# Performance work log

Hardware: AMD Instinct MI355X
Metric: run time of the kernel (lower is better)

Reference implementation:

```python
import jax, jax.numpy as jnp
import numpy as np
from jax import lax

RADIUS = 0.3
NSAMPLE = 16
NPOINT = 1024
NH = 1   # num_heading_bin
NS = 18  # num_size_cluster
EPS = 1e-5  # torch BatchNorm eps


def _bn(x, g, b, m, v):
    # eval-mode batchnorm over the last (channel) axis
    return (x - m) * (g / jnp.sqrt(v + EPS)) + b


def _fps(xyz, npoint):
    # furthest point sampling; xyz: (B,K,3) -> (B,npoint) int32 indices
    B, K, _ = xyz.shape
    def body(carry, _):
        dists, far = carry
        cur = jnp.take_along_axis(xyz, far[:, None, None], axis=1)  # (B,1,3)
        d = jnp.sum((xyz - cur) ** 2, -1)                           # (B,K)
        dists = jnp.minimum(dists, d)
        nxt = jnp.argmax(dists, -1).astype(jnp.int32)
        return (dists, nxt), far
    init = (jnp.full((B, K), 1e10, xyz.dtype), jnp.zeros((B,), jnp.int32))
    _, inds = lax.scan(body, init, None, length=npoint)
    return jnp.swapaxes(inds, 0, 1)  # (B, npoint)


def _ball_query(xyz, new_xyz):
    # first-NSAMPLE points within RADIUS of each center, pad with first hit
    K = xyz.shape[1]
    d2 = jnp.sum((new_xyz[:, :, None, :] - xyz[:, None, :, :]) ** 2, -1)  # (B,S,K)
    mask = d2 < RADIUS ** 2
    idx = jnp.where(mask, jnp.arange(K, dtype=jnp.int32)[None, None, :], K)
    idx = jnp.sort(idx, -1)[..., :NSAMPLE]
    first = idx[..., :1]
    idx = jnp.where(idx == K, first, idx)
    idx = jnp.where(idx == K, 0, idx)  # degenerate: no neighbor at all
    return idx  # (B,S,NSAMPLE)


def setup_inputs() -> dict:
    key = jax.random.key(0)
    ks = jax.random.split(key, 32)
    inp = {}
    inp['xyz'] = jax.random.normal(ks[0], (8, 8192, 3), jnp.float32)
    inp['features'] = jax.random.normal(ks[1], (8, 256, 8192), jnp.float32)
    i = 2
    # shared MLP: 259 -> 128 -> 128 -> 128 (conv2d 1x1, no bias, then BN)
    for l, (o, c) in enumerate([(128, 259), (128, 128), (128, 128)]):
        inp[f'mlp_w{l}'] = jax.random.normal(ks[i], (o, c), jnp.float32) * 0.1; i += 1
        inp[f'mlp_g{l}'] = jnp.ones((o,), jnp.float32)
        inp[f'mlp_b{l}'] = jnp.zeros((o,), jnp.float32)
        inp[f'mlp_m{l}'] = jax.random.normal(ks[i], (o,), jnp.float32) * 0.01; i += 1
        inp[f'mlp_v{l}'] = jax.random.uniform(ks[i], (o,), jnp.float32, 0.5, 1.5); i += 1
    # box head convs (conv1d k=1)
    for nm, (o, c) in [('c1', (128, 128)), ('c2', (128, 128)), ('c3', (97, 128))]:
        inp[f'{nm}_w'] = jax.random.normal(ks[i], (o, c), jnp.float32) * 0.1; i += 1
        inp[f'{nm}_b'] = jnp.zeros((o,), jnp.float32)
    for nm in ['bn1', 'bn2']:
        inp[f'{nm}_g'] = jnp.ones((128,), jnp.float32)
        inp[f'{nm}_b'] = jnp.zeros((128,), jnp.float32)
        inp[f'{nm}_m'] = jax.random.normal(ks[i], (128,), jnp.float32) * 0.01; i += 1
        inp[f'{nm}_v'] = jax.random.uniform(ks[i], (128,), jnp.float32, 0.5, 1.5); i += 1
    inp['mean_size_arr'] = jax.random.uniform(ks[i], (NS, 3), jnp.float32, 0.3, 2.0)
    return inp


def reference(xyz, features,
              mlp_w0, mlp_g0, mlp_b0, mlp_m0, mlp_v0,
              mlp_w1, mlp_g1, mlp_b1, mlp_m1, mlp_v1,
              mlp_w2, mlp_g2, mlp_b2, mlp_m2, mlp_v2,
              c1_w, c1_b, bn1_g, bn1_b, bn1_m, bn1_v,
              c2_w, c2_b, bn2_g, bn2_b, bn2_m, bn2_v,
              c3_w, c3_b, mean_size_arr):
    B = xyz.shape[0]
    # --- vote aggregation: FPS + ball query + group + shared MLP + maxpool ---
    fps_inds = _fps(xyz, NPOINT)
    new_xyz = jnp.take_along_axis(xyz, fps_inds[..., None], axis=1)  # (B,S,3)
    idx = _ball_query(xyz, new_xyz)                                  # (B,S,n)
    gather = jax.vmap(lambda a, i: a[i])
    g_xyz = (gather(xyz, idx) - new_xyz[:, :, None, :]) / RADIUS     # normalize_xyz
    g_f = gather(jnp.swapaxes(features, 1, 2), idx)                  # (B,S,n,256)
    h = jnp.concatenate([g_xyz, g_f], -1)                            # (B,S,n,259)
    for w, g, b, m, v in ((mlp_w0, mlp_g0, mlp_b0, mlp_m0, mlp_v0),
                          (mlp_w1, mlp_g1, mlp_b1, mlp_m1, mlp_v1),
                          (mlp_w2, mlp_g2, mlp_b2, mlp_m2, mlp_v2)):
        h = jax.nn.relu(_bn(jnp.einsum('bsnc,oc->bsno', h, w), g, b, m, v))
    feat = jnp.max(h, axis=2)                                        # (B,S,128)
    # --- box head (conv1d k=1 == per-point linear) ---
    net = jax.nn.relu(_bn(jnp.einsum('bsc,oc->bso', feat, c1_w) + c1_b,
                          bn1_g, bn1_b, bn1_m, bn1_v))
    net = jax.nn.relu(_bn(jnp.einsum('bsc,oc->bso', net, c2_w) + c2_b,
                          bn2_g, bn2_b, bn2_m, bn2_v))
    net = jnp.einsum('bsc,oc->bso', net, c3_w) + c3_b                # (B,S,97)
    # --- decode_scores ---
    obj = net[..., 0:2]
    center = new_xyz + net[..., 2:5]
    hs = net[..., 5:5 + NH]
    hr = net[..., 5 + NH:5 + 2 * NH] * (np.pi / NH)
    ss = net[..., 5 + 2 * NH:5 + 2 * NH + NS]
    srn = net[..., 5 + 2 * NH + NS:5 + 2 * NH + 4 * NS].reshape(B, NPOINT, NS, 3)
    sr = (srn * mean_size_arr[None, None]).reshape(B, NPOINT, NS * 3)
    sem = net[..., 5 + 2 * NH + 4 * NS:]
    return jnp.concatenate([obj, center, hs, hr, ss, sr, sem], -1)   # (B,S,97)
```

## Files before the change

### kernel.cpp

```cpp
#include <hip/hip_runtime.h>
#include <cstdint>
#include <cstddef>

#define BATCH   8
#define KPTS    8192
#define NPT     1024
#define NSAMP   16
#define RAD2    0.09f

typedef float f32x2 __attribute__((ext_vector_type(2)));
typedef float f32x4 __attribute__((ext_vector_type(4)));
typedef short s16x4 __attribute__((ext_vector_type(4)));
typedef short s16x8 __attribute__((ext_vector_type(8)));

__device__ __forceinline__ unsigned short f2bf(float x) {
    unsigned u = __float_as_uint(x);
    return (unsigned short)((u + 0x7fffu + ((u >> 16) & 1u)) >> 16);
}

template <int CTRL>
__device__ __forceinline__ unsigned long long dpp_max_step(unsigned long long v) {
    unsigned int lo = (unsigned int)v, hi = (unsigned int)(v >> 32);
    unsigned int lo2 = (unsigned int)__builtin_amdgcn_update_dpp(0, (int)lo, CTRL, 0xf, 0xf, true);
    unsigned int hi2 = (unsigned int)__builtin_amdgcn_update_dpp(0, (int)hi, CTRL, 0xf, 0xf, true);
    unsigned long long o = ((unsigned long long)hi2 << 32) | lo2;
    return o > v ? o : v;
}

__global__ __launch_bounds__(512, 1) void fps_f0_kernel(
    const float* __restrict__ xyz, float* __restrict__ new_xyz,
    const float* __restrict__ feats, const float* __restrict__ w0,
    float* __restrict__ f0out) {
    __shared__ float xs[KPTS], ys[KPTS], zs[KPTS];
    __shared__ __align__(16) unsigned long long wslot[2][8];
    __shared__ int   hist[NPT];
    __shared__ float As[16 * 128];
    __shared__ float Bs[16 * 130];

    const int tid = threadIdx.x;

    if (blockIdx.x >= 8) {
        const int bid = blockIdx.x - 8;
        const int b   = bid >> 6;
        const int p0  = (bid & 63) << 7;
        const int rb  = (tid >> 4) << 2;
        const int ob  = tid & 15;
        const float* fb = feats + (size_t)b * 256 * KPTS;

        float acc[4][8];
#pragma unroll
        for (int r = 0; r < 4; ++r)
#pragma unroll
            for (int c = 0; c < 8; ++c) acc[r][c] = 0.f;

        for (int k0 = 0; k0 < 256; k0 += 16) {
#pragma unroll
            for (int i = 0; i < 4; ++i) {
                int e = tid + (i << 9);
                int kk = e >> 7, pc = e & 127;
                As[kk * 128 + pc] = fb[(size_t)(k0 + kk) * KPTS + p0 + pc];
            }
#pragma unroll
            for (int i = 0; i < 4; ++i) {
                int e = tid + (i << 9);
                int o = e >> 4, kk = e & 15;
                Bs[kk * 130 + o] = w0[o * 259 + 3 + k0 + kk];
            }
            __syncthreads();
#pragma unroll
            for (int kk = 0; kk < 16; ++kk) {
                float a[4], wvv[8];
#pragma unroll
                for (int r = 0; r < 4; ++r) a[r] = As[kk * 128 + rb + r];
#pragma unroll
                for (int c = 0; c < 8; ++c) wvv[c] = Bs[kk * 130 + ob + (c << 4)];
#pragma unroll
                for (int r = 0; r < 4; ++r)
#pragma unroll
                    for (int c = 0; c < 8; ++c) acc[r][c] = fmaf(a[r], wvv[c], acc[r][c]);
            }
            __syncthreads();
        }
#pragma unroll
        for (int r = 0; r < 4; ++r) {
            float* outp = f0out + ((size_t)b * KPTS + p0 + rb + r) * 128 + ob;
#pragma unroll
            for (int c = 0; c < 8; ++c) outp[c << 4] = acc[r][c];
        }
        return;
    }

    {
#pragma clang fp contract(off)
        const int b = blockIdx.x;
        const float* xb = xyz + (size_t)b * KPTS * 3;

        for (int i = tid; i < KPTS; i += 512) {
            xs[i] = xb[i * 3 + 0];
            ys[i] = xb[i * 3 + 1];
            zs[i] = xb[i * 3 + 2];
        }
        __syncthreads();

        const int base = tid << 4;
        f32x2 px[8], py[8], pz[8], dmn[8];
#pragma unroll
        for (int j = 0; j < 8; ++j) {
            int i0 = base + (j << 1);
            px[j] = (f32x2){xs[i0], xs[i0 + 1]};
            py[j] = (f32x2){ys[i0], ys[i0 + 1]};
            pz[j] = (f32x2){zs[i0], zs[i0 + 1]};
            dmn[j] = (f32x2){1e10f, 1e10f};
        }

        int far = 0;
        for (int it = 0; it < NPT; ++it) {
            if (tid == 0) hist[it] = far;
            const float cx = xs[far], cy = ys[far], cz = zs[far];
            const f32x2 cx2 = (f32x2){cx, cx};
            const f32x2 cy2 = (f32x2){cy, cy};
            const f32x2 cz2 = (f32x2){cz, cz};

            f32x2 mm = (f32x2){-1.0f, -1.0f};
#pragma unroll
            for (int j = 0; j < 8; ++j) {
                f32x2 dx = px[j] - cx2;
                f32x2 dy = py[j] - cy2;
                f32x2 dz = pz[j] - cz2;
                f32x2 d  = (dx * dx + dy * dy) + dz * dz;
                f32x2 nd = __builtin_elementwise_min(dmn[j], d);
                dmn[j] = nd;
                mm = __builtin_elementwise_max(mm, nd);
            }
            float lmax = fmaxf(mm.x, mm.y);

            int ci = 0x7fffffff;
#pragma unroll
            for (int j = 0; j < 8; ++j) {
                if (dmn[j].x == lmax) ci = min(ci, base + (j << 1));
                if (dmn[j].y == lmax) ci = min(ci, base + (j << 1) + 1);
            }

            unsigned long long pk =
                ((unsigned long long)__float_as_uint(lmax) << 32) | (unsigned)(8191 - ci);

            pk = dpp_max_step<0x111>(pk);
            pk = dpp_max_step<0x112>(pk);
            pk = dpp_max_step<0x114>(pk);
            pk = dpp_max_step<0x118>(pk);
            pk = dpp_max_step<0x142>(pk);
            pk = dpp_max_step<0x143>(pk);

            if ((tid & 63) == 63) wslot[it & 1][tid >> 6] = pk;
            __syncthreads();

            ulonglong2 s01 = *(const ulonglong2*)&wslot[it & 1][0];
            ulonglong2 s23 = *(const ulonglong2*)&wslot[it & 1][2];
            ulonglong2 s45 = *(const ulonglong2*)&wslot[it & 1][4];
            ulonglong2 s67 = *(const ulonglong2*)&wslot[it & 1][6];
            unsigned long long g = s01.x;
            if (s01.y > g) g = s01.y;
            if (s23.x > g) g = s23.x;
            if (s23.y > g) g = s23.y;
            if (s45.x > g) g = s45.x;
            if (s45.y > g) g = s45.y;
            if (s67.x > g) g = s67.x;
            if (s67.y > g) g = s67.y;
            far = 8191 - (int)(unsigned)(g & 0xffffffffull);
        }

        for (int i = tid; i < NPT; i += 512) {
            int idx = hist[i];
            float* o = new_xyz + ((size_t)b * NPT + i) * 3;
            o[0] = xs[idx]; o[1] = ys[idx]; o[2] = zs[idx];
        }
    }
}

__global__ __launch_bounds__(256) void ballq_kernel(const float* __restrict__ xyz,
                                                    const float* __restrict__ new_xyz,
                                                    int* __restrict__ idxout) {
    const int tid  = threadIdx.x;
    const int lane = tid & 63;
    const int q    = (blockIdx.x << 2) + (tid >> 6);
    const int b    = q >> 10;
    const float* xb = xyz + (size_t)b * KPTS * 3;
    const float qx = new_xyz[q * 3 + 0];
    const float qy = new_xyz[q * 3 + 1];
    const float qz = new_xyz[q * 3 + 2];
    int* op = idxout + q * NSAMP;

    int total = 0;
    int first_p = 0;
    for (int c = 0; c < KPTS / 64; ++c) {
        int p = (c << 6) + lane;
        float pxv = xb[p * 3 + 0], pyv = xb[p * 3 + 1], pzv = xb[p * 3 + 2];
        float dx = __fsub_rn(qx, pxv), dy = __fsub_rn(qy, pyv), dz = __fsub_rn(qz, pzv);
        float d2 = __fadd_rn(__fadd_rn(__fmul_rn(dx, dx), __fmul_rn(dy, dy)),
                             __fmul_rn(dz, dz));
        bool pred = d2 < RAD2;
        unsigned long long mask = __ballot(pred);
        if (total == 0 && mask != 0ull) first_p = (c << 6) + (int)__builtin_ctzll(mask);
        if (pred) {
            int rank = (int)__popcll(mask & ((1ull << lane) - 1ull));
            int slot = total + rank;
            if (slot < NSAMP) op[slot] = p;
        }
        total += (int)__popcll(mask);
        if (total >= NSAMP) break;
    }
    if (total < NSAMP && lane >= total && lane < NSAMP) op[lane] = first_p;
}

#define HB 136

__global__ __launch_bounds__(256) void mlp_kernel(
    const float* __restrict__ f0, const int* __restrict__ idxw,
    const float* __restrict__ xyz, const float* __restrict__ new_xyz,
    const float* __restrict__ w0,
    const float* __restrict__ g0, const float* __restrict__ b0,
    const float* __restrict__ m0, const float* __restrict__ v0,
    const float* __restrict__ w1,
    const float* __restrict__ g1, const float* __restrict__ b1a,
    const float* __restrict__ m1, const float* __restrict__ v1,
    const float* __restrict__ w2,
    const float* __restrict__ g2, const float* __restrict__ b2a,
    const float* __restrict__ m2, const float* __restrict__ v2,
    float* __restrict__ featout) {
    const int tid = threadIdx.x;
    const int q0  = blockIdx.x << 2;
    const int b   = q0 >> 10;

    __shared__ __align__(16) unsigned short hbf[64 * HB];
    __shared__ __align__(16) unsigned short Wsh[128 * HB];
    __shared__ float gx[64], gy[64], gz[64];
    __shared__ int   pidx[64];
    __shared__ float s0[128], t0[128], wxs[128], wys[128], wzs[128];
    __shared__ float s1[128], t1[128], s2[128], t2[128];

    if (tid < 64) pidx[tid] = idxw[(q0 + (tid >> 4)) * NSAMP + (tid & 15)];
    if (tid < 128) {
        float sc = g0[tid] / sqrtf(v0[tid] + 1e-5f);
        s0[tid] = sc; t0[tid] = b0[tid] - m0[tid] * sc;
        sc = g1[tid] / sqrtf(v1[tid] + 1e-5f);
        s1[tid] = sc; t1[tid] = b1a[tid] - m1[tid] * sc;
        sc = g2[tid] / sqrtf(v2[tid] + 1e-5f);
        s2[tid] = sc; t2[tid] = b2a[tid] - m2[tid] * sc;
        wxs[tid] = w0[tid * 259 + 0];
        wys[tid] = w0[tid * 259 + 1];
        wzs[tid] = w0[tid * 259 + 2];
    }
    __syncthreads();
    if (tid < 64) {
        int p = pidx[tid];
        int q = q0 + (tid >> 4);
        const float* pp = xyz + ((size_t)b * KPTS + p) * 3;
        const float* nq = new_xyz + (size_t)q * 3;
        gx[tid] = (pp[0] - nq[0]) / 0.3f;
        gy[tid] = (pp[1] - nq[1]) / 0.3f;
        gz[tid] = (pp[2] - nq[2]) / 0.3f;
    }
    __syncthreads();

#pragma unroll 2
    for (int i = 0; i < 8; ++i) {
        int e = tid + (i << 8);
        int row = e >> 5, o = (e & 31) << 2;
        int p = pidx[row];
        float4 v4 = *(const float4*)(f0 + ((size_t)b * KPTS + p) * 128 + o);
        float gxr = gx[row], gyr = gy[row], gzr = gz[row];
        float r0 = fmaf(wzs[o + 0], gzr, fmaf(wys[o + 0], gyr, fmaf(wxs[o + 0], gxr, v4.x)));
        float r1 = fmaf(wzs[o + 1], gzr, fmaf(wys[o + 1], gyr, fmaf(wxs[o + 1], gxr, v4.y)));
        float r2 = fmaf(wzs[o + 2], gzr, fmaf(wys[o + 2], gyr, fmaf(wxs[o + 2], gxr, v4.z)));
        float r3 = fmaf(wzs[o + 3], gzr, fmaf(wys[o + 3], gyr, fmaf(wxs[o + 3], gxr, v4.w)));
        s16x4 c4;
        c4.x = (short)f2bf(fmaxf(fmaf(r0, s0[o + 0], t0[o + 0]), 0.f));
        c4.y = (short)f2bf(fmaxf(fmaf(r1, s0[o + 1], t0[o + 1]), 0.f));
        c4.z = (short)f2bf(fmaxf(fmaf(r2, s0[o + 2], t0[o + 2]), 0.f));
        c4.w = (short)f2bf(fmaxf(fmaf(r3, s0[o + 3], t0[o + 3]), 0.f));
        *(s16x4*)&hbf[row * HB + o] = c4;
    }
#pragma unroll 4
    for (int i = 0; i < 16; ++i) {
        int e = tid + (i << 8);
        int o = e >> 5;
        int kt = (e & 31) << 2;
        float4 w4 = *(const float4*)(w1 + o * 128 + kt);
        s16x4 c4 = { (short)f2bf(w4.x), (short)f2bf(w4.y),
                     (short)f2bf(w4.z), (short)f2bf(w4.w) };
        *(s16x4*)&Wsh[o * HB + kt] = c4;
    }
    __syncthreads();

    const int w    = tid >> 6;
    const int lane = tid & 63;
    const int l15  = lane & 15;
    const int quad = lane >> 4;
    const int wrow = w << 4;

    f32x4 acc[8];
#pragma unroll
    for (int t = 0; t < 8; ++t) acc[t] = (f32x4){0.f, 0.f, 0.f, 0.f};
#pragma unroll
    for (int k0 = 0; k0 < 128; k0 += 32) {
        s16x8 a = *(const s16x8*)&hbf[(wrow + l15) * HB + k0 + (quad << 3)];
#pragma unroll
        for (int t = 0; t < 8; ++t) {
            s16x8 bf = *(const s16x8*)&Wsh[((t << 4) + l15) * HB + k0 + (quad << 3)];
            acc[t] = __builtin_amdgcn_mfma_f32_16x16x32_bf16(a, bf, acc[t], 0, 0, 0);
        }
    }
    __syncthreads();

#pragma unroll
    for (int t = 0; t < 8; ++t) {
        int o = (t << 4) + l15;
        float ss = s1[o], tt = t1[o];
#pragma unroll
        for (int r = 0; r < 4; ++r) {
            float v = fmaxf(fmaf(acc[t][r], ss, tt), 0.f);
            hbf[(wrow + (quad << 2) + r) * HB + o] = f2bf(v);
        }
    }
#pragma unroll 4
    for (int i = 0; i < 16; ++i) {
        int e = tid + (i << 8);
        int o = e >> 5;
        int kt = (e & 31) << 2;
        float4 w4 = *(const float4*)(w2 + o * 128 + kt);
        s16x4 c4 = { (short)f2bf(w4.x), (short)f2bf(w4.y),
                     (short)f2bf(w4.z), (short)f2bf(w4.w) };
        *(s16x4*)&Wsh[o * HB + kt] = c4;
    }
    __syncthreads();

#pragma unroll
    for (int t = 0; t < 8; ++t) acc[t] = (f32x4){0.f, 0.f, 0.f, 0.f};
#pragma unroll
    for (int k0 = 0; k0 < 128; k0 += 32) {
        s16x8 a = *(const s16x8*)&hbf[(wrow + l15) * HB + k0 + (quad << 3)];
#pragma unroll
        for (int t = 0; t < 8; ++t) {
            s16x8 bf = *(const s16x8*)&Wsh[((t << 4) + l15) * HB + k0 + (quad << 3)];
            acc[t] = __builtin_amdgcn_mfma_f32_16x16x32_bf16(a, bf, acc[t], 0, 0, 0);
        }
    }

#pragma unroll
    for (int t = 0; t < 8; ++t) {
        int o = (t << 4) + l15;
        float ss = s2[o], tt = t2[o];
        float m0v = fmaxf(fmaf(acc[t][0], ss, tt), 0.f);
        float m1v = fmaxf(fmaf(acc[t][1], ss, tt), 0.f);
        float m2v = fmaxf(fmaf(acc[t][2], ss, tt), 0.f);
        float m3v = fmaxf(fmaf(acc[t][3], ss, tt), 0.f);
        float m = fmaxf(fmaxf(m0v, m1v), fmaxf(m2v, m3v));
        m = fmaxf(m, __shfl_xor(m, 16));
        m = fmaxf(m, __shfl_xor(m, 32));
        if (quad == 0)
            featout[(size_t)(q0 + w) * 128 + o] = m;
    }
}

__global__ __launch_bounds__(256) void head_kernel(
    const float* __restrict__ feat, const float* __restrict__ new_xyz,
    const float* __restrict__ c1w, const float* __restrict__ c1b,
    const float* __restrict__ c2w, const float* __restrict__ c2b,
    const float* __restrict__ c3w, const float* __restrict__ c3b,
    const float* __restrict__ bg1, const float* __restrict__ bb1,
    const float* __restrict__ bm1, const float* __restrict__ bv1,
    const float* __restrict__ bg2, const float* __restrict__ bb2,
    const float* __restrict__ bm2, const float* __restrict__ bv2,
    const float* __restrict__ msz, float* __restrict__ out) {
    const int tid = threadIdx.x;
    const int q0  = blockIdx.x << 3;
    __shared__ float fs[8][128], n1[8][128], n2[8][128];
    __shared__ float s1[128], t1[128], s2[128], t2[128], ms[54];

#pragma unroll
    for (int i = 0; i < 4; ++i) {
        int e = tid + (i << 8);
        fs[e >> 7][e & 127] = feat[(size_t)q0 * 128 + e];
    }
    if (tid < 128) {
        float sc = bg1[tid] / sqrtf(bv1[tid] + 1e-5f);
        s1[tid] = sc; t1[tid] = bb1[tid] - bm1[tid] * sc;
        sc = bg2[tid] / sqrtf(bv2[tid] + 1e-5f);
        s2[tid] = sc; t2[tid] = bb2[tid] - bm2[tid] * sc;
    }
    if (tid < 54) ms[tid] = msz[tid];
    __syncthreads();

    const int o    = tid & 127;
    const int half = tid >> 7;

    {
        float a[4];
#pragma unroll
        for (int j = 0; j < 4; ++j) a[j] = c1b[o];
        const float* wr = c1w + o * 128;
        for (int k = 0; k < 128; k += 4) {
            float4 w4 = *(const float4*)(wr + k);
#pragma unroll
            for (int j = 0; j < 4; ++j) {
                int qq = half * 4 + j;
                a[j] = fmaf(fs[qq][k + 0], w4.x, a[j]);
                a[j] = fmaf(fs[qq][k + 1], w4.y, a[j]);
                a[j] = fmaf(fs[qq][k + 2], w4.z, a[j]);
                a[j] = fmaf(fs[qq][k + 3], w4.w, a[j]);
            }
        }
#pragma unroll
        for (int j = 0; j < 4; ++j)
            n1[half * 4 + j][o] = fmaxf(fmaf(a[j], s1[o], t1[o]), 0.f);
    }
    __syncthreads();
    {
        float a[4];
#pragma unroll
        for (int j = 0; j < 4; ++j) a[j] = c2b[o];
        const float* wr = c2w + o * 128;
        for (int k = 0; k < 128; k += 4) {
            float4 w4 = *(const float4*)(wr + k);
#pragma unroll
            for (int j = 0; j < 4; ++j) {
                int qq = half * 4 + j;
                a[j] = fmaf(n1[qq][k + 0], w4.x, a[j]);
                a[j] = fmaf(n1[qq][k + 1], w4.y, a[j]);
                a[j] = fmaf(n1[qq][k + 2], w4.z, a[j]);
                a[j] = fmaf(n1[qq][k + 3], w4.w, a[j]);
            }
        }
#pragma unroll
        for (int j = 0; j < 4; ++j)
            n2[half * 4 + j][o] = fmaxf(fmaf(a[j], s2[o], t2[o]), 0.f);
    }
    __syncthreads();
    if (o < 97) {
        float a[4];
#pragma unroll
        for (int j = 0; j < 4; ++j) a[j] = c3b[o];
        const float* wr = c3w + o * 128;
        for (int k = 0; k < 128; k += 4) {
            float4 w4 = *(const float4*)(wr + k);
#pragma unroll
            for (int j = 0; j < 4; ++j) {
                int qq = half * 4 + j;
                a[j] = fmaf(n2[qq][k + 0], w4.x, a[j]);
                a[j] = fmaf(n2[qq][k + 1], w4.y, a[j]);
                a[j] = fmaf(n2[qq][k + 2], w4.z, a[j]);
                a[j] = fmaf(n2[qq][k + 3], w4.w, a[j]);
            }
        }
#pragma unroll
        for (int j = 0; j < 4; ++j) {
            int q = q0 + half * 4 + j;
            float v = a[j];
            if (o >= 2 && o < 5) v += new_xyz[(size_t)q * 3 + (o - 2)];
            else if (o == 6) v *= 3.14159265358979323846f;
            else if (o >= 25 && o < 79) v *= ms[o - 25];
            out[(size_t)q * 97 + o] = v;
        }
    }
}

extern "C" void kernel_launch(void* const* d_in, const int* in_sizes, int n_in,
                              void* d_out, int out_size, void* d_ws, size_t ws_size,
                              hipStream_t stream) {
    const float* xyz      = (const float*)d_in[0];
    const float* features = (const float*)d_in[1];
    const float* w0  = (const float*)d_in[2];
    const float* g0  = (const float*)d_in[3];
    const float* b0  = (const float*)d_in[4];
    const float* m0  = (const float*)d_in[5];
    const float* v0  = (const float*)d_in[6];
    const float* w1  = (const float*)d_in[7];
    const float* g1  = (const float*)d_in[8];
    const float* b1  = (const float*)d_in[9];
    const float* m1  = (const float*)d_in[10];
    const float* v1  = (const float*)d_in[11];
    const float* w2  = (const float*)d_in[12];
    const float* g2  = (const float*)d_in[13];
    const float* b2  = (const float*)d_in[14];
    const float* m2  = (const float*)d_in[15];
    const float* v2  = (const float*)d_in[16];
    const float* c1w = (const float*)d_in[17];
    const float* c1b = (const float*)d_in[18];
    const float* c2w = (const float*)d_in[19];
    const float* c2b = (const float*)d_in[20];
    const float* c3w = (const float*)d_in[21];
    const float* c3b = (const float*)d_in[22];
    const float* bg1 = (const float*)d_in[23];
    const float* bb1 = (const float*)d_in[24];
    const float* bm1 = (const float*)d_in[25];
    const float* bv1 = (const float*)d_in[26];
    const float* bg2 = (const float*)d_in[27];
    const float* bb2 = (const float*)d_in[28];
    const float* bm2 = (const float*)d_in[29];
    const float* bv2 = (const float*)d_in[30];
    const float* msz = (const float*)d_in[31];

    float* F0   = (float*)d_ws;
    float* feat = F0 + (size_t)BATCH * KPTS * 128;
    int*   idxw = (int*)(feat + (size_t)BATCH * NPT * 128);
    float* nxyz = (float*)(idxw + (size_t)BATCH * NPT * NSAMP);
    float* outp = (float*)d_out;

    fps_f0_kernel<<<8 + BATCH * (KPTS / 128), 512, 0, stream>>>(
        xyz, nxyz, features, w0, F0);
    ballq_kernel<<<BATCH * NPT / 4, 256, 0, stream>>>(xyz, nxyz, idxw);
    mlp_kernel  <<<BATCH * NPT / 4, 256, 0, stream>>>(
        F0, idxw, xyz, nxyz, w0, g0, b0, m0, v0,
        w1, g1, b1, m1, v1, w2, g2, b2, m2, v2, feat);
    head_kernel <<<BATCH * NPT / 8, 256, 0, stream>>>(
        feat, nxyz, c1w, c1b, c2w, c2b, c3w, c3b,
        bg1, bb1, bm1, bv1, bg2, bb2, bm2, bv2, msz, outp);
}
```

Before: 1.248 ms.

## Shrink FPS block to 256 threads, reduce argmax via float DPP and LDS atomicMax

```diff
diff --git a/kernel.cpp b/kernel.cpp
--- a/kernel.cpp
+++ b/kernel.cpp
@@ -19,30 +19,27 @@
 }
 
 template <int CTRL>
-__device__ __forceinline__ unsigned long long dpp_max_step(unsigned long long v) {
-    unsigned int lo = (unsigned int)v, hi = (unsigned int)(v >> 32);
-    unsigned int lo2 = (unsigned int)__builtin_amdgcn_update_dpp(0, (int)lo, CTRL, 0xf, 0xf, true);
-    unsigned int hi2 = (unsigned int)__builtin_amdgcn_update_dpp(0, (int)hi, CTRL, 0xf, 0xf, true);
-    unsigned long long o = ((unsigned long long)hi2 << 32) | lo2;
-    return o > v ? o : v;
-}
-
-__global__ __launch_bounds__(512, 1) void fps_f0_kernel(
+__device__ __forceinline__ float dppmaxf(float v) {
+    int o = __builtin_amdgcn_update_dpp(0, __float_as_int(v), CTRL, 0xf, 0xf, true);
+    return fmaxf(v, __int_as_float(o));
+}
+
+__global__ __launch_bounds__(256, 1) void fps_f0_kernel(
     const float* __restrict__ xyz, float* __restrict__ new_xyz,
     const float* __restrict__ feats, const float* __restrict__ w0,
     float* __restrict__ f0out) {
     __shared__ float xs[KPTS], ys[KPTS], zs[KPTS];
-    __shared__ __align__(16) unsigned long long wslot[2][8];
+    __shared__ unsigned long long slot3[3];
     __shared__ int   hist[NPT];
-    __shared__ float As[16 * 128];
+    __shared__ float As[16 * 64];
     __shared__ float Bs[16 * 130];
 
     const int tid = threadIdx.x;
 
     if (blockIdx.x >= 8) {
         const int bid = blockIdx.x - 8;
-        const int b   = bid >> 6;
-        const int p0  = (bid & 63) << 7;
+        const int b   = bid >> 7;
+        const int p0  = (bid & 127) << 6;
         const int rb  = (tid >> 4) << 2;
         const int ob  = tid & 15;
         const float* fb = feats + (size_t)b * 256 * KPTS;
@@ -56,13 +53,13 @@
         for (int k0 = 0; k0 < 256; k0 += 16) {
 #pragma unroll
             for (int i = 0; i < 4; ++i) {
-                int e = tid + (i << 9);
-                int kk = e >> 7, pc = e & 127;
-                As[kk * 128 + pc] = fb[(size_t)(k0 + kk) * KPTS + p0 + pc];
-            }
-#pragma unroll
-            for (int i = 0; i < 4; ++i) {
-                int e = tid + (i << 9);
+                int e = tid + (i << 8);
+                int kk = e >> 6, pc = e & 63;
+                As[kk * 64 + pc] = fb[(size_t)(k0 + kk) * KPTS + p0 + pc];
+            }
+#pragma unroll
+            for (int i = 0; i < 8; ++i) {
+                int e = tid + (i << 8);
                 int o = e >> 4, kk = e & 15;
                 Bs[kk * 130 + o] = w0[o * 259 + 3 + k0 + kk];
             }
@@ -71,7 +68,7 @@
             for (int kk = 0; kk < 16; ++kk) {
                 float a[4], wvv[8];
 #pragma unroll
-                for (int r = 0; r < 4; ++r) a[r] = As[kk * 128 + rb + r];
+                for (int r = 0; r < 4; ++r) a[r] = As[kk * 64 + rb + r];
 #pragma unroll
                 for (int c = 0; c < 8; ++c) wvv[c] = Bs[kk * 130 + ob + (c << 4)];
 #pragma unroll
@@ -95,17 +92,18 @@
         const int b = blockIdx.x;
         const float* xb = xyz + (size_t)b * KPTS * 3;
 
-        for (int i = tid; i < KPTS; i += 512) {
+        for (int i = tid; i < KPTS; i += 256) {
             xs[i] = xb[i * 3 + 0];
             ys[i] = xb[i * 3 + 1];
             zs[i] = xb[i * 3 + 2];
         }
+        if (tid < 3) slot3[tid] = 0ull;
         __syncthreads();
 
-        const int base = tid << 4;
-        f32x2 px[8], py[8], pz[8], dmn[8];
-#pragma unroll
-        for (int j = 0; j < 8; ++j) {
+        const int base = tid << 5;
+        f32x2 px[16], py[16], pz[16], dmn[16];
+#pragma unroll
+        for (int j = 0; j < 16; ++j) {
             int i0 = base + (j << 1);
             px[j] = (f32x2){xs[i0], xs[i0 + 1]};
             py[j] = (f32x2){ys[i0], ys[i0 + 1]};
@@ -113,9 +111,11 @@
             dmn[j] = (f32x2){1e10f, 1e10f};
         }
 
+        const int lane = tid & 63;
         int far = 0;
+        int cur = 0, nxt = 1;
         for (int it = 0; it < NPT; ++it) {
-            if (tid == 0) hist[it] = far;
+            if (tid == 0) { hist[it] = far; slot3[nxt] = 0ull; }
             const float cx = xs[far], cy = ys[far], cz = zs[far];
             const f32x2 cx2 = (f32x2){cx, cx};
             const f32x2 cy2 = (f32x2){cy, cy};
@@ -123,7 +123,7 @@
 
             f32x2 mm = (f32x2){-1.0f, -1.0f};
 #pragma unroll
-            for (int j = 0; j < 8; ++j) {
+            for (int j = 0; j < 16; ++j) {
                 f32x2 dx = px[j] - cx2;
                 f32x2 dy = py[j] - cy2;
                 f32x2 dz = pz[j] - cz2;
@@ -136,40 +136,40 @@
 
             int ci = 0x7fffffff;
 #pragma unroll
-            for (int j = 0; j < 8; ++j) {
+            for (int j = 0; j < 16; ++j) {
                 if (dmn[j].x == lmax) ci = min(ci, base + (j << 1));
                 if (dmn[j].y == lmax) ci = min(ci, base + (j << 1) + 1);
             }
 
-            unsigned long long pk =
-                ((unsigned long long)__float_as_uint(lmax) << 32) | (unsigned)(8191 - ci);
-
-            pk = dpp_max_step<0x111>(pk);
-            pk = dpp_max_step<0x112>(pk);
-            pk = dpp_max_step<0x114>(pk);
-            pk = dpp_max_step<0x118>(pk);
-            pk = dpp_max_step<0x142>(pk);
-            pk = dpp_max_step<0x143>(pk);
-
-            if ((tid & 63) == 63) wslot[it & 1][tid >> 6] = pk;
+            float wm = lmax;
+            wm = dppmaxf<0x111>(wm);
+            wm = dppmaxf<0x112>(wm);
+            wm = dppmaxf<0x114>(wm);
+            wm = dppmaxf<0x118>(wm);
+            wm = dppmaxf<0x142>(wm);
+            wm = dppmaxf<0x143>(wm);
+            float wmax = __int_as_float(
+                __builtin_amdgcn_readlane(__float_as_int(wm), 63));
+
+            unsigned long long mk = __ballot(lmax == wmax);
+            int wl = (int)__builtin_ctzll(mk);
+            int cw = __builtin_amdgcn_readlane(ci, wl);
+
+            if (lane == 0) {
+                unsigned long long pk =
+                    ((unsigned long long)__float_as_uint(wmax) << 32)
+                    | (unsigned)(8191 - cw);
+                atomicMax(&slot3[cur], pk);
+            }
             __syncthreads();
 
-            ulonglong2 s01 = *(const ulonglong2*)&wslot[it & 1][0];
-            ulonglong2 s23 = *(const ulonglong2*)&wslot[it & 1][2];
-            ulonglong2 s45 = *(const ulonglong2*)&wslot[it & 1][4];
-            ulonglong2 s67 = *(const ulonglong2*)&wslot[it & 1][6];
-            unsigned long long g = s01.x;
-            if (s01.y > g) g = s01.y;
-            if (s23.x > g) g = s23.x;
-            if (s23.y > g) g = s23.y;
-            if (s45.x > g) g = s45.x;
-            if (s45.y > g) g = s45.y;
-            if (s67.x > g) g = s67.x;
-            if (s67.y > g) g = s67.y;
+            unsigned long long g = slot3[cur];
             far = 8191 - (int)(unsigned)(g & 0xffffffffull);
-        }
-
-        for (int i = tid; i < NPT; i += 512) {
+            cur = nxt;
+            nxt = (nxt == 2) ? 0 : nxt + 1;
+        }
+
+        for (int i = tid; i < NPT; i += 256) {
             int idx = hist[i];
             float* o = new_xyz + ((size_t)b * NPT + i) * 3;
             o[0] = xs[idx]; o[1] = ys[idx]; o[2] = zs[idx];
@@ -506,7 +506,7 @@
     float* nxyz = (float*)(idxw + (size_t)BATCH * NPT * NSAMP);
     float* outp = (float*)d_out;
 
-    fps_f0_kernel<<<8 + BATCH * (KPTS / 128), 512, 0, stream>>>(
+    fps_f0_kernel<<<8 + BATCH * (KPTS / 64), 256, 0, stream>>>(
         xyz, nxyz, features, w0, F0);
     ballq_kernel<<<BATCH * NPT / 4, 256, 0, stream>>>(xyz, nxyz, idxw);
     mlp_kernel  <<<BATCH * NPT / 4, 256, 0, stream>>>(
```

Measured after the change: 1.233 ms. About the same (-1.2%).
